# Optimization experiments

Measured on AMD Instinct MI355X. Metric: run time of the kernel, lower is better.

Reference implementation:

```python
import jax, jax.numpy as jnp
import numpy as np

T, B = 512, 64
DIM_INPUT, DIM_LATENT, VOCAB = 512, 1024, 50257


def setup_inputs() -> dict:
    key = jax.random.key(0)
    ks = jax.random.split(key, 12)
    s = 0.02
    return {
        "X": jax.random.randint(ks[0], (T, B), 0, VOCAB, dtype=jnp.int32),
        "h": jax.random.normal(ks[1], (B, DIM_LATENT), dtype=jnp.float32),
        "emb": jax.random.normal(ks[2], (VOCAB, DIM_INPUT), dtype=jnp.float32) * s,
        "Wf": jax.random.normal(ks[3], (DIM_LATENT + DIM_INPUT, DIM_LATENT), dtype=jnp.float32) * s,
        "bf": jnp.zeros((DIM_LATENT,), dtype=jnp.float32),
        "Wi": jax.random.normal(ks[4], (DIM_LATENT + DIM_INPUT, DIM_LATENT), dtype=jnp.float32) * s,
        "bi": jnp.zeros((DIM_LATENT,), dtype=jnp.float32),
        "Wc": jax.random.normal(ks[5], (DIM_LATENT + DIM_INPUT, DIM_LATENT), dtype=jnp.float32) * s,
        "bc": jnp.zeros((DIM_LATENT,), dtype=jnp.float32),
        "Wo": jax.random.normal(ks[6], (DIM_LATENT + DIM_INPUT, DIM_LATENT), dtype=jnp.float32) * s,
        "bo": jnp.zeros((DIM_LATENT,), dtype=jnp.float32),
    }


def reference(X, h, emb, Wf, bf, Wi, bi, Wc, bc, Wo, bo):
    # X: [T, B] int tokens; h: [B, dim_latent]
    xe = emb[X]  # [T, B, dim_input] embedding gather
    c0 = jnp.zeros_like(h)

    def step(carry, x_t):
        h_prev, c_prev = carry
        m = jnp.concatenate([h_prev, x_t], axis=1)  # [B, dl+di]
        ft = jax.nn.sigmoid(m @ Wf + bf)
        it = jax.nn.sigmoid(m @ Wi + bi)
        ct = ft * c_prev + it * jnp.tanh(m @ Wc + bc)
        ot = jax.nn.sigmoid(m @ Wo + bo)
        ht = ot * jnp.tanh(ct)
        return (ht, ct), ht

    (_, _), H = jax.lax.scan(step, (h, c0), xe)
    return H  # [T, B, dim_latent]
```

## Files before the change

### kernel.cpp

```cpp
#include <hip/hip_runtime.h>


namespace {
constexpr int T_STEPS = 512;
constexpr int BATCH   = 64;
constexpr int DI      = 512;
constexpr int DL      = 1024;
constexpr int NKC     = 48;
constexpr int NKC_H   = 32;
constexpr int NBLK    = 256;
constexpr int NTHR    = 320;
constexpr int FPAD    = 32;
constexpr int EPOCH_IDX = NBLK * FPAD;
}

typedef __attribute__((ext_vector_type(8))) short bf16x8;
typedef __attribute__((ext_vector_type(8))) unsigned short u16x8;
typedef __attribute__((ext_vector_type(4))) float f32x4;
typedef __attribute__((ext_vector_type(4))) unsigned int u32x4;
typedef __attribute__((ext_vector_type(2))) unsigned int u32x2;

__device__ __forceinline__ unsigned short f2bf(float x){
  unsigned int u = __float_as_uint(x);
  return (unsigned short)((u + 0x7FFFu + ((u >> 16) & 1u)) >> 16);
}
__device__ __forceinline__ float bf2f(unsigned short b){
  return __uint_as_float(((unsigned int)b) << 16);
}
__device__ __forceinline__ float fast_sigmoid(float v){
  return __fdividef(1.f, 1.f + __expf(-v));
}
__device__ __forceinline__ float fast_tanh(float v){
  v = fminf(fmaxf(v, -15.f), 15.f);
  float t = __expf(2.f * v);
  return __fdividef(t - 1.f, t + 1.f);
}

__global__ void prep_xe(const int* __restrict__ X, const float* __restrict__ emb,
                        unsigned short* __restrict__ xe){
  int i = blockIdx.x * blockDim.x + threadIdx.x;
  const int total = T_STEPS * BATCH * DI / 8;
  if (i >= total) return;
  int row = i >> 6;
  int seg = i & 63;
  int tok = X[row];
  const float* src = emb + (long long)tok * DI + seg * 8;
  float4 v0 = *(const float4*)src;
  float4 v1 = *(const float4*)(src + 4);
  u16x8 o;
  o[0]=f2bf(v0.x); o[1]=f2bf(v0.y); o[2]=f2bf(v0.z); o[3]=f2bf(v0.w);
  o[4]=f2bf(v1.x); o[5]=f2bf(v1.y); o[6]=f2bf(v1.z); o[7]=f2bf(v1.w);
  *(u16x8*)(xe + (long long)row * DI + seg * 8) = o;
}

__global__ void prep_w(const float* __restrict__ Wf, const float* __restrict__ Wi,
                       const float* __restrict__ Wc, const float* __restrict__ Wo,
                       unsigned short* __restrict__ W_hi, unsigned short* __restrict__ W_lo){
  int idx = blockIdx.x * blockDim.x + threadIdx.x;
  if (idx >= 256 * NKC * 64) return;
  int lane = idx & 63;
  int kc   = (idx >> 6) % NKC;
  int bk   = idx / (64 * NKC);
  int lc = lane & 15, kg = lane >> 4;
  int g  = lc >> 2;
  int jl = bk * 4 + (lc & 3);
  const float* Wg = (g == 0) ? Wf : ((g == 1) ? Wi : ((g == 2) ? Wc : Wo));
  int kbase = kc * 32 + kg * 8;
  u16x8 hi, lo;
#pragma unroll
  for (int j = 0; j < 8; j++){
    float wv = Wg[(long long)(kbase + j) * DL + jl];
    unsigned short h = f2bf(wv);
    hi[j] = h;
    lo[j] = f2bf(wv - bf2f(h));
  }
  *(u16x8*)(W_hi + ((long long)(bk * NKC + kc) * 64 + lane) * 8) = hi;
  if (kc < NKC_H)
    *(u16x8*)(W_lo + ((long long)(bk * NKC_H + kc) * 64 + lane) * 8) = lo;
}

__global__ void prep_h(const float* __restrict__ h0,
                       const float* __restrict__ bf_, const float* __restrict__ bi_,
                       const float* __restrict__ bc_, const float* __restrict__ bo_,
                       unsigned short* __restrict__ hRing,
                       float* __restrict__ bias_pack, unsigned int* __restrict__ bar){
  int i = blockIdx.x * blockDim.x + threadIdx.x;
  if (i < BATCH * DL) hRing[i] = f2bf(h0[i]);
  if (i < 4096){
    int r = i & 3, g = (i >> 2) & 3, bk = i >> 4;
    const float* bg = (g == 0) ? bf_ : ((g == 1) ? bi_ : ((g == 2) ? bc_ : bo_));
    bias_pack[i] = bg[bk * 4 + r];
  }
  if (i < (NBLK + 1) * FPAD) bar[i] = 0u;
}

template<bool CACHED>
__launch_bounds__(NTHR, 1)
__global__ void lstm_persist(const unsigned short* __restrict__ xe,
                             const unsigned short* __restrict__ W_hi,
                             const unsigned short* __restrict__ W_lo,
                             unsigned short* __restrict__ hRing,
                             const float* __restrict__ bias_pack,
                             float* __restrict__ out,
                             unsigned int* __restrict__ bar){
  extern __shared__ unsigned short lds[];
  unsigned short* lds_hi = lds;
  unsigned short* lds_lo = lds + NKC * 512;
  __shared__ unsigned short stage_h[BATCH * 4];
  __shared__ float          stage_o[BATCH * 4];
  const int tid  = threadIdx.x;
  const int bk   = blockIdx.x;
  const int w    = tid >> 6;
  const int lane = tid & 63;
  const bool isAgg     = (bk == 0) && (w == 4);
  const bool isCompute = (w < 4);

  const uint4* srcHi = (const uint4*)(W_hi + (size_t)bk * NKC * 512);
  uint4* dHi = (uint4*)lds_hi;
  for (int i = tid; i < 3072; i += NTHR) dHi[i] = srcHi[i];
  const uint4* srcLo = (const uint4*)(W_lo + (size_t)bk * NKC_H * 512);
  uint4* dLo = (uint4*)lds_lo;
  for (int i = tid; i < 2048; i += NTHR) dLo[i] = srcLo[i];
  __syncthreads();

  const int lc = lane & 15;
  const int kg = lane >> 4;
  const int g  = lc >> 2;
  const int rowb = (w << 4) + lc;
  const float bias = bias_pack[bk * 16 + lc];
  const int srcBase = (lane & 48) | (lc & 3);
  const int hOff = rowb * DL + kg * 8;
  const int xOff = rowb * DI + kg * 8;
  unsigned int* epochp = bar + EPOCH_IDX;
  float cr0 = 0.f, cr1 = 0.f, cr2 = 0.f, cr3 = 0.f;

  f32x4 acc0 = {0.f,0.f,0.f,0.f}, acc1 = {0.f,0.f,0.f,0.f};
  f32x4 acc2 = {0.f,0.f,0.f,0.f}, acc3 = {0.f,0.f,0.f,0.f};

#define XSTEP(KC, ACC) {                                                        \
    bf16x8 ax = *(const bf16x8*)(xRow + (KC) * 32);                             \
    bf16x8 bh = *(const bf16x8*)(lds_hi + (NKC_H + (KC)) * 512 + lane * 8);     \
    ACC = __builtin_amdgcn_mfma_f32_16x16x32_bf16(ax, bh, ACC, 0, 0, 0); }
#define HSTEP2(KC, ACC) {                                                       \
    bf16x8 ah = *(const bf16x8*)&hv[KC];                                        \
    bf16x8 bh = *(const bf16x8*)(lds_hi + (KC) * 512 + lane * 8);               \
    bf16x8 bl = *(const bf16x8*)(lds_lo + (KC) * 512 + lane * 8);               \
    ACC = __builtin_amdgcn_mfma_f32_16x16x32_bf16(ah, bh, ACC, 0, 0, 0);        \
    ACC = __builtin_amdgcn_mfma_f32_16x16x32_bf16(ah, bl, ACC, 0, 0, 0); }
#define LOADHC(I, OFFSTR)                                                       \
    asm volatile("global_load_dwordx4 %0, %1, off offset:" OFFSTR               \
                 : "=v"(hv[I]) : "v"(hbase));
#define LOADHU(I, OFFSTR)                                                       \
    asm volatile("global_load_dwordx4 %0, %1, off offset:" OFFSTR " sc0 sc1"    \
                 : "=v"(hv[I]) : "v"(hbase));

  if (isCompute){
    const unsigned short* xRow = xe + xOff;
#pragma unroll
    for (int kc = 0; kc < 16; kc += 4){
      XSTEP(kc, acc0) XSTEP(kc + 1, acc1) XSTEP(kc + 2, acc2) XSTEP(kc + 3, acc3)
    }
  }

#pragma unroll 1
  for (int t = 0; t < T_STEPS; ++t){
    if (t > 0){
      if (isAgg){
        const unsigned tgt = (unsigned)t;
        int spin = 0;
        for (;;){
          unsigned v0 = __hip_atomic_load(bar + (lane      ) * FPAD, __ATOMIC_RELAXED, __HIP_MEMORY_SCOPE_AGENT);
          unsigned v1 = __hip_atomic_load(bar + (lane +  64) * FPAD, __ATOMIC_RELAXED, __HIP_MEMORY_SCOPE_AGENT);
          unsigned v2 = __hip_atomic_load(bar + (lane + 128) * FPAD, __ATOMIC_RELAXED, __HIP_MEMORY_SCOPE_AGENT);
          unsigned v3 = __hip_atomic_load(bar + (lane + 192) * FPAD, __ATOMIC_RELAXED, __HIP_MEMORY_SCOPE_AGENT);
          bool ok = (v0 >= tgt) & (v1 >= tgt) & (v2 >= tgt) & (v3 >= tgt);
          if (__all(ok ? 1 : 0)) break;
          __builtin_amdgcn_s_sleep(1);
          if (++spin > (1 << 15)) break;
        }
        if (lane == 0)
          __hip_atomic_store(epochp, tgt, __ATOMIC_RELAXED, __HIP_MEMORY_SCOPE_AGENT);
      } else if (w == 0){
        const unsigned tgt = (unsigned)t;
        int spin = 0;
        while (__hip_atomic_load(epochp, __ATOMIC_RELAXED, __HIP_MEMORY_SCOPE_AGENT) < tgt){
          __builtin_amdgcn_s_sleep(1);
          if (++spin > (1 << 16)) break;
        }
      }
    }
    __syncthreads();

    const int slotR = CACHED ? t       : (t & 1);
    const int slotW = CACHED ? (t + 1) : ((t + 1) & 1);
    unsigned short* hWr = hRing + (size_t)slotW * (BATCH * DL);
    float* out_t = out + (size_t)t * (BATCH * DL);

    if (isCompute){
      u32x4 hv[32];
      const unsigned short* hbase = hRing + (size_t)slotR * (BATCH * DL) + hOff;
      if constexpr (CACHED){
        LOADHC( 0,"0")    LOADHC( 1,"64")   LOADHC( 2,"128")  LOADHC( 3,"192")
        LOADHC( 4,"256")  LOADHC( 5,"320")  LOADHC( 6,"384")  LOADHC( 7,"448")
        LOADHC( 8,"512")  LOADHC( 9,"576")  LOADHC(10,"640")  LOADHC(11,"704")
        LOADHC(12,"768")  LOADHC(13,"832")  LOADHC(14,"896")  LOADHC(15,"960")
        LOADHC(16,"1024") LOADHC(17,"1088") LOADHC(18,"1152") LOADHC(19,"1216")
        LOADHC(20,"1280") LOADHC(21,"1344") LOADHC(22,"1408") LOADHC(23,"1472")
        LOADHC(24,"1536") LOADHC(25,"1600") LOADHC(26,"1664") LOADHC(27,"1728")
        LOADHC(28,"1792") LOADHC(29,"1856") LOADHC(30,"1920") LOADHC(31,"1984")
      } else {
        LOADHU( 0,"0")    LOADHU( 1,"64")   LOADHU( 2,"128")  LOADHU( 3,"192")
        LOADHU( 4,"256")  LOADHU( 5,"320")  LOADHU( 6,"384")  LOADHU( 7,"448")
        LOADHU( 8,"512")  LOADHU( 9,"576")  LOADHU(10,"640")  LOADHU(11,"704")
        LOADHU(12,"768")  LOADHU(13,"832")  LOADHU(14,"896")  LOADHU(15,"960")
        LOADHU(16,"1024") LOADHU(17,"1088") LOADHU(18,"1152") LOADHU(19,"1216")
        LOADHU(20,"1280") LOADHU(21,"1344") LOADHU(22,"1408") LOADHU(23,"1472")
        LOADHU(24,"1536") LOADHU(25,"1600") LOADHU(26,"1664") LOADHU(27,"1728")
        LOADHU(28,"1792") LOADHU(29,"1856") LOADHU(30,"1920") LOADHU(31,"1984")
      }
      asm volatile("s_waitcnt vmcnt(0)" ::: "memory");
      __builtin_amdgcn_sched_barrier(0);

#pragma unroll
      for (int kc = 0; kc < NKC_H; kc += 4){
        HSTEP2(kc, acc0) HSTEP2(kc + 1, acc1) HSTEP2(kc + 2, acc2) HSTEP2(kc + 3, acc3)
      }
      f32x4 acc = (acc0 + acc1) + (acc2 + acc3);

      float creg[4] = {cr0, cr1, cr2, cr3};
#pragma unroll
      for (int r = 0; r < 4; r++){
        float v = acc[r] + bias;
        float vF = __shfl(v, srcBase);
        float vI = __shfl(v, srcBase + 4);
        float vC = __shfl(v, srcBase + 8);
        float vO = __shfl(v, srcBase + 12);
        if (g == 0){
          int b = (w << 4) | (kg << 2) | r;
          float ft = fast_sigmoid(vF);
          float it = fast_sigmoid(vI);
          float gt = fast_tanh(vC);
          float ot = fast_sigmoid(vO);
          float cn = ft * creg[r] + it * gt;
          creg[r] = cn;
          float hn = ot * fast_tanh(cn);
          int si = (b << 2) | (lc & 3);
          stage_h[si] = f2bf(hn);
          stage_o[si] = hn;
        }
      }
      cr0 = creg[0]; cr1 = creg[1]; cr2 = creg[2]; cr3 = creg[3];
    }

    __syncthreads();

    if (w == 0){
      u32x2  hv2 = *(const u32x2*)&stage_h[lane << 2];
      f32x4  ov  = *(const f32x4*)&stage_o[lane << 2];
      *(float4*)(out_t + lane * DL + (bk << 2)) = *(const float4*)&ov;
      unsigned short* hdst = hWr + lane * DL + (bk << 2);
      asm volatile("global_store_dwordx2 %0, %1, off sc0 sc1"
                   :: "v"(hdst), "v"(hv2) : "memory");
      asm volatile("s_waitcnt vmcnt(0)" ::: "memory");
      __builtin_amdgcn_sched_barrier(0);
      if (tid == 0)
        __hip_atomic_store(bar + bk * FPAD, (unsigned)(t + 1),
                           __ATOMIC_RELAXED, __HIP_MEMORY_SCOPE_AGENT);
    }

    acc0 = (f32x4){0.f,0.f,0.f,0.f}; acc1 = (f32x4){0.f,0.f,0.f,0.f};
    acc2 = (f32x4){0.f,0.f,0.f,0.f}; acc3 = (f32x4){0.f,0.f,0.f,0.f};
    if (isCompute && t + 1 < T_STEPS){
      const unsigned short* xRow = xe + (size_t)(t + 1) * BATCH * DI + xOff;
#pragma unroll
      for (int kc = 0; kc < 16; kc += 4){
        XSTEP(kc, acc0) XSTEP(kc + 1, acc1) XSTEP(kc + 2, acc2) XSTEP(kc + 3, acc3)
      }
    }
  }
#undef XSTEP
#undef HSTEP2
#undef LOADHC
#undef LOADHU
}

extern "C" void kernel_launch(void* const* d_in, const int* in_sizes, int n_in,
                              void* d_out, int out_size, void* d_ws, size_t ws_size,
                              hipStream_t stream){
  const int*   X   = (const int*)d_in[0];
  const float* h0  = (const float*)d_in[1];
  const float* emb = (const float*)d_in[2];
  const float* Wf  = (const float*)d_in[3];
  const float* bf_ = (const float*)d_in[4];
  const float* Wi  = (const float*)d_in[5];
  const float* bi_ = (const float*)d_in[6];
  const float* Wc  = (const float*)d_in[7];
  const float* bc_ = (const float*)d_in[8];
  const float* Wo  = (const float*)d_in[9];
  const float* bo_ = (const float*)d_in[10];
  float* out = (float*)d_out;

  const size_t SLOT = (size_t)BATCH * DL;
  const size_t base_need =
      sizeof(unsigned short) * ((size_t)T_STEPS * BATCH * DI
                              + (size_t)256 * NKC * 512
                              + (size_t)256 * NKC_H * 512)
    + sizeof(float) * 4096
    + sizeof(unsigned int) * (NBLK + 1) * FPAD + 4096;
  const size_t ring_full = sizeof(unsigned short) * SLOT * (size_t)(T_STEPS + 1);
  const bool cached = ws_size >= base_need + ring_full;
  const size_t ring_elems = cached ? SLOT * (size_t)(T_STEPS + 1) : SLOT * 2;

  char* ws = (char*)d_ws;
  size_t off = 0;
  auto alloc = [&](size_t bytes) -> void* {
    void* p = ws + off;
    off = (off + bytes + 255) & ~((size_t)255);
    return p;
  };
  unsigned short* xe        = (unsigned short*)alloc(sizeof(unsigned short) * (size_t)T_STEPS * BATCH * DI);
  unsigned short* W_hi      = (unsigned short*)alloc(sizeof(unsigned short) * (size_t)256 * NKC * 512);
  unsigned short* W_lo      = (unsigned short*)alloc(sizeof(unsigned short) * (size_t)256 * NKC_H * 512);
  unsigned short* hRing     = (unsigned short*)alloc(sizeof(unsigned short) * ring_elems);
  float*          bias_pack = (float*)alloc(sizeof(float) * 4096);
  unsigned int*   bar       = (unsigned int*)alloc(sizeof(unsigned int) * (NBLK + 1) * FPAD);
  (void)in_sizes; (void)n_in; (void)out_size;

  static bool attr_set = false;
  if (!attr_set){
    hipFuncSetAttribute((const void*)lstm_persist<true>,
                        hipFuncAttributeMaxDynamicSharedMemorySize, 160 * 1024);
    hipFuncSetAttribute((const void*)lstm_persist<false>,
                        hipFuncAttributeMaxDynamicSharedMemorySize, 160 * 1024);
    attr_set = true;
  }

  hipLaunchKernelGGL(prep_xe, dim3(8192), dim3(256), 0, stream, X, emb, xe);
  hipLaunchKernelGGL(prep_w,  dim3(3072), dim3(256), 0, stream, Wf, Wi, Wc, Wo, W_hi, W_lo);
  hipLaunchKernelGGL(prep_h,  dim3(256),  dim3(256), 0, stream, h0, bf_, bi_, bc_, bo_,
                     hRing, bias_pack, bar);
  if (cached)
    hipLaunchKernelGGL((lstm_persist<true>),  dim3(NBLK), dim3(NTHR), 80 * 1024, stream,
                       xe, W_hi, W_lo, hRing, bias_pack, out, bar);
  else
    hipLaunchKernelGGL((lstm_persist<false>), dim3(NBLK), dim3(NTHR), 80 * 1024, stream,
                       xe, W_hi, W_lo, hRing, bias_pack, out, bar);
}
```

Measured before the change: 4.355 ms.

## Use a dedicated store/barrier wave with LDS counter instead of block syncs

Wave 4 becomes a dedicated communicator: it waits on an LDS atomic counter that the compute waves bump, then stores h and the output and publishes the per-block flag. Block 0's wave 4 also aggregates the grid barrier. Compute waves no longer run __syncthreads; they only spin on the epoch word, so the output store and barrier overlap with the next step's x-projection. The h ring layout changes to a block-major slot (bk, batch, 4) so each store is contiguous, with loads reshaped as paired dwordx2 reads. This relies on correct workgroup fence ordering between the compute waves and the communicator wave.

```diff
diff --git a/kernel.cpp b/kernel.cpp
--- a/kernel.cpp
+++ b/kernel.cpp
@@ -11,7 +11,9 @@
 constexpr int NBLK    = 256;
 constexpr int NTHR    = 320;
 constexpr int FPAD    = 32;
-constexpr int EPOCH_IDX = NBLK * FPAD;
+constexpr int EPOCH_IDX   = NBLK * FPAD;
+constexpr int SLOT_ELEMS  = NBLK * BATCH * 4;
+constexpr int SLOT_BYTES  = SLOT_ELEMS * 2;
 }
 
 typedef __attribute__((ext_vector_type(8))) short bf16x8;
@@ -85,7 +87,13 @@
                        unsigned short* __restrict__ hRing,
                        float* __restrict__ bias_pack, unsigned int* __restrict__ bar){
   int i = blockIdx.x * blockDim.x + threadIdx.x;
-  if (i < BATCH * DL) hRing[i] = f2bf(h0[i]);
+  if (i < NBLK * BATCH){
+    int bk = i >> 6, b = i & 63;
+    float4 v = *(const float4*)(h0 + (size_t)b * DL + (bk << 2));
+    u16x8* dummy; (void)dummy;
+    unsigned short* d = hRing + (size_t)i * 4;
+    d[0] = f2bf(v.x); d[1] = f2bf(v.y); d[2] = f2bf(v.z); d[3] = f2bf(v.w);
+  }
   if (i < 4096){
     int r = i & 3, g = (i >> 2) & 3, bk = i >> 4;
     const float* bg = (g == 0) ? bf_ : ((g == 1) ? bi_ : ((g == 2) ? bc_ : bo_));
@@ -108,12 +116,11 @@
   unsigned short* lds_lo = lds + NKC * 512;
   __shared__ unsigned short stage_h[BATCH * 4];
   __shared__ float          stage_o[BATCH * 4];
+  __shared__ unsigned int   cnt1;
   const int tid  = threadIdx.x;
   const int bk   = blockIdx.x;
   const int w    = tid >> 6;
   const int lane = tid & 63;
-  const bool isAgg     = (bk == 0) && (w == 4);
-  const bool isCompute = (w < 4);
 
   const uint4* srcHi = (const uint4*)(W_hi + (size_t)bk * NKC * 512);
   uint4* dHi = (uint4*)lds_hi;
@@ -121,7 +128,60 @@
   const uint4* srcLo = (const uint4*)(W_lo + (size_t)bk * NKC_H * 512);
   uint4* dLo = (uint4*)lds_lo;
   for (int i = tid; i < 2048; i += NTHR) dLo[i] = srcLo[i];
+  if (tid == 0) cnt1 = 0u;
   __syncthreads();
+
+  unsigned int* epochp = bar + EPOCH_IDX;
+
+  if (w == 4){
+#pragma unroll 1
+    for (int t = 0; t < T_STEPS; ++t){
+      {
+        const unsigned tgt = 4u * (unsigned)(t + 1);
+        int sp = 0;
+        while (__hip_atomic_load(&cnt1, __ATOMIC_RELAXED, __HIP_MEMORY_SCOPE_WORKGROUP) < tgt){
+          if (++sp > (1 << 22)) break;
+        }
+      }
+      __builtin_amdgcn_fence(__ATOMIC_ACQUIRE, "workgroup");
+
+      const int slotW = CACHED ? (t + 1) : ((t + 1) & 1);
+      u32x2 hv2 = *(const u32x2*)&stage_h[lane << 2];
+      f32x4 ov  = *(const f32x4*)&stage_o[lane << 2];
+      unsigned long long sbR = (unsigned long long)hRing
+                             + (unsigned long long)slotW * SLOT_BYTES + (unsigned)(bk << 9);
+      unsigned voR = (unsigned)(lane << 3);
+      unsigned long long sbO = (unsigned long long)(out + (size_t)t * (BATCH * DL) + (bk << 2));
+      unsigned voO = (unsigned)(lane << 12);
+      asm volatile("global_store_dwordx2 %0, %1, %2 sc0 sc1"
+                   :: "v"(voR), "v"(hv2), "s"(sbR) : "memory");
+      asm volatile("global_store_dwordx4 %0, %1, %2"
+                   :: "v"(voO), "v"(ov), "s"(sbO) : "memory");
+      asm volatile("s_waitcnt vmcnt(1)" ::: "memory");
+      __builtin_amdgcn_sched_barrier(0);
+      if (lane == 0)
+        __hip_atomic_store(bar + bk * FPAD, (unsigned)(t + 1),
+                           __ATOMIC_RELAXED, __HIP_MEMORY_SCOPE_AGENT);
+
+      if (bk == 0 && t + 1 < T_STEPS){
+        const unsigned tg2 = (unsigned)(t + 1);
+        int sp = 0;
+        for (;;){
+          unsigned v0 = __hip_atomic_load(bar + (lane      ) * FPAD, __ATOMIC_RELAXED, __HIP_MEMORY_SCOPE_AGENT);
+          unsigned v1 = __hip_atomic_load(bar + (lane +  64) * FPAD, __ATOMIC_RELAXED, __HIP_MEMORY_SCOPE_AGENT);
+          unsigned v2 = __hip_atomic_load(bar + (lane + 128) * FPAD, __ATOMIC_RELAXED, __HIP_MEMORY_SCOPE_AGENT);
+          unsigned v3 = __hip_atomic_load(bar + (lane + 192) * FPAD, __ATOMIC_RELAXED, __HIP_MEMORY_SCOPE_AGENT);
+          bool ok = (v0 >= tg2) & (v1 >= tg2) & (v2 >= tg2) & (v3 >= tg2);
+          if (__all(ok ? 1 : 0)) break;
+          __builtin_amdgcn_s_sleep(1);
+          if (++sp > (1 << 15)) break;
+        }
+        if (lane == 0)
+          __hip_atomic_store(epochp, tg2, __ATOMIC_RELAXED, __HIP_MEMORY_SCOPE_AGENT);
+      }
+    }
+    return;
+  }
 
   const int lc = lane & 15;
   const int kg = lane >> 4;
@@ -129,9 +189,8 @@
   const int rowb = (w << 4) + lc;
   const float bias = bias_pack[bk * 16 + lc];
   const int srcBase = (lane & 48) | (lc & 3);
-  const int hOff = rowb * DL + kg * 8;
+  const unsigned laneoff = (unsigned)(kg * 1024 + rowb * 8);
   const int xOff = rowb * DI + kg * 8;
-  unsigned int* epochp = bar + EPOCH_IDX;
   float cr0 = 0.f, cr1 = 0.f, cr2 = 0.f, cr3 = 0.f;
 
   f32x4 acc0 = {0.f,0.f,0.f,0.f}, acc1 = {0.f,0.f,0.f,0.f};
@@ -141,20 +200,28 @@
     bf16x8 ax = *(const bf16x8*)(xRow + (KC) * 32);                             \
     bf16x8 bh = *(const bf16x8*)(lds_hi + (NKC_H + (KC)) * 512 + lane * 8);     \
     ACC = __builtin_amdgcn_mfma_f32_16x16x32_bf16(ax, bh, ACC, 0, 0, 0); }
+#define LOADH(KC) { unsigned vo = laneoff + (KC) * 4096u;                       \
+    if constexpr (CACHED){                                                      \
+      asm volatile("global_load_dwordx2 %0, %2, %3\n\t"                         \
+                   "global_load_dwordx2 %1, %2, %3 offset:512"                  \
+                   : "=&v"(hv[(KC)*2]), "=&v"(hv[(KC)*2+1])                     \
+                   : "v"(vo), "s"(sb));                                         \
+    } else {                                                                    \
+      asm volatile("global_load_dwordx2 %0, %2, %3 sc0 sc1\n\t"                 \
+                   "global_load_dwordx2 %1, %2, %3 offset:512 sc0 sc1"          \
+                   : "=&v"(hv[(KC)*2]), "=&v"(hv[(KC)*2+1])                     \
+                   : "v"(vo), "s"(sb));                                         \
+    } }
 #define HSTEP2(KC, ACC) {                                                       \
-    bf16x8 ah = *(const bf16x8*)&hv[KC];                                        \
+    u32x4 av; av[0] = hv[(KC)*2][0]; av[1] = hv[(KC)*2][1];                     \
+    av[2] = hv[(KC)*2+1][0]; av[3] = hv[(KC)*2+1][1];                           \
+    bf16x8 ah = *(bf16x8*)&av;                                                  \
     bf16x8 bh = *(const bf16x8*)(lds_hi + (KC) * 512 + lane * 8);               \
     bf16x8 bl = *(const bf16x8*)(lds_lo + (KC) * 512 + lane * 8);               \
     ACC = __builtin_amdgcn_mfma_f32_16x16x32_bf16(ah, bh, ACC, 0, 0, 0);        \
     ACC = __builtin_amdgcn_mfma_f32_16x16x32_bf16(ah, bl, ACC, 0, 0, 0); }
-#define LOADHC(I, OFFSTR)                                                       \
-    asm volatile("global_load_dwordx4 %0, %1, off offset:" OFFSTR               \
-                 : "=v"(hv[I]) : "v"(hbase));
-#define LOADHU(I, OFFSTR)                                                       \
-    asm volatile("global_load_dwordx4 %0, %1, off offset:" OFFSTR " sc0 sc1"    \
-                 : "=v"(hv[I]) : "v"(hbase));
-
-  if (isCompute){
+
+  {
     const unsigned short* xRow = xe + xOff;
 #pragma unroll
     for (int kc = 0; kc < 16; kc += 4){
@@ -165,112 +232,64 @@
 #pragma unroll 1
   for (int t = 0; t < T_STEPS; ++t){
     if (t > 0){
-      if (isAgg){
-        const unsigned tgt = (unsigned)t;
-        int spin = 0;
-        for (;;){
-          unsigned v0 = __hip_atomic_load(bar + (lane      ) * FPAD, __ATOMIC_RELAXED, __HIP_MEMORY_SCOPE_AGENT);
-          unsigned v1 = __hip_atomic_load(bar + (lane +  64) * FPAD, __ATOMIC_RELAXED, __HIP_MEMORY_SCOPE_AGENT);
-          unsigned v2 = __hip_atomic_load(bar + (lane + 128) * FPAD, __ATOMIC_RELAXED, __HIP_MEMORY_SCOPE_AGENT);
-          unsigned v3 = __hip_atomic_load(bar + (lane + 192) * FPAD, __ATOMIC_RELAXED, __HIP_MEMORY_SCOPE_AGENT);
-          bool ok = (v0 >= tgt) & (v1 >= tgt) & (v2 >= tgt) & (v3 >= tgt);
-          if (__all(ok ? 1 : 0)) break;
-          __builtin_amdgcn_s_sleep(1);
-          if (++spin > (1 << 15)) break;
-        }
-        if (lane == 0)
-          __hip_atomic_store(epochp, tgt, __ATOMIC_RELAXED, __HIP_MEMORY_SCOPE_AGENT);
-      } else if (w == 0){
-        const unsigned tgt = (unsigned)t;
-        int spin = 0;
-        while (__hip_atomic_load(epochp, __ATOMIC_RELAXED, __HIP_MEMORY_SCOPE_AGENT) < tgt){
-          __builtin_amdgcn_s_sleep(1);
-          if (++spin > (1 << 16)) break;
-        }
-      }
-    }
-    __syncthreads();
-
-    const int slotR = CACHED ? t       : (t & 1);
-    const int slotW = CACHED ? (t + 1) : ((t + 1) & 1);
-    unsigned short* hWr = hRing + (size_t)slotW * (BATCH * DL);
-    float* out_t = out + (size_t)t * (BATCH * DL);
-
-    if (isCompute){
-      u32x4 hv[32];
-      const unsigned short* hbase = hRing + (size_t)slotR * (BATCH * DL) + hOff;
-      if constexpr (CACHED){
-        LOADHC( 0,"0")    LOADHC( 1,"64")   LOADHC( 2,"128")  LOADHC( 3,"192")
-        LOADHC( 4,"256")  LOADHC( 5,"320")  LOADHC( 6,"384")  LOADHC( 7,"448")
-        LOADHC( 8,"512")  LOADHC( 9,"576")  LOADHC(10,"640")  LOADHC(11,"704")
-        LOADHC(12,"768")  LOADHC(13,"832")  LOADHC(14,"896")  LOADHC(15,"960")
-        LOADHC(16,"1024") LOADHC(17,"1088") LOADHC(18,"1152") LOADHC(19,"1216")
-        LOADHC(20,"1280") LOADHC(21,"1344") LOADHC(22,"1408") LOADHC(23,"1472")
-        LOADHC(24,"1536") LOADHC(25,"1600") LOADHC(26,"1664") LOADHC(27,"1728")
-        LOADHC(28,"1792") LOADHC(29,"1856") LOADHC(30,"1920") LOADHC(31,"1984")
-      } else {
-        LOADHU( 0,"0")    LOADHU( 1,"64")   LOADHU( 2,"128")  LOADHU( 3,"192")
-        LOADHU( 4,"256")  LOADHU( 5,"320")  LOADHU( 6,"384")  LOADHU( 7,"448")
-        LOADHU( 8,"512")  LOADHU( 9,"576")  LOADHU(10,"640")  LOADHU(11,"704")
-        LOADHU(12,"768")  LOADHU(13,"832")  LOADHU(14,"896")  LOADHU(15,"960")
-        LOADHU(16,"1024") LOADHU(17,"1088") LOADHU(18,"1152") LOADHU(19,"1216")
-        LOADHU(20,"1280") LOADHU(21,"1344") LOADHU(22,"1408") LOADHU(23,"1472")
-        LOADHU(24,"1536") LOADHU(25,"1600") LOADHU(26,"1664") LOADHU(27,"1728")
-        LOADHU(28,"1792") LOADHU(29,"1856") LOADHU(30,"1920") LOADHU(31,"1984")
-      }
-      asm volatile("s_waitcnt vmcnt(0)" ::: "memory");
-      __builtin_amdgcn_sched_barrier(0);
-
-#pragma unroll
-      for (int kc = 0; kc < NKC_H; kc += 4){
-        HSTEP2(kc, acc0) HSTEP2(kc + 1, acc1) HSTEP2(kc + 2, acc2) HSTEP2(kc + 3, acc3)
-      }
-      f32x4 acc = (acc0 + acc1) + (acc2 + acc3);
-
-      float creg[4] = {cr0, cr1, cr2, cr3};
-#pragma unroll
-      for (int r = 0; r < 4; r++){
-        float v = acc[r] + bias;
-        float vF = __shfl(v, srcBase);
-        float vI = __shfl(v, srcBase + 4);
-        float vC = __shfl(v, srcBase + 8);
-        float vO = __shfl(v, srcBase + 12);
-        if (g == 0){
-          int b = (w << 4) | (kg << 2) | r;
-          float ft = fast_sigmoid(vF);
-          float it = fast_sigmoid(vI);
-          float gt = fast_tanh(vC);
-          float ot = fast_sigmoid(vO);
-          float cn = ft * creg[r] + it * gt;
-          creg[r] = cn;
-          float hn = ot * fast_tanh(cn);
-          int si = (b << 2) | (lc & 3);
-          stage_h[si] = f2bf(hn);
-          stage_o[si] = hn;
-        }
-      }
-      cr0 = creg[0]; cr1 = creg[1]; cr2 = creg[2]; cr3 = creg[3];
-    }
-
-    __syncthreads();
-
-    if (w == 0){
-      u32x2  hv2 = *(const u32x2*)&stage_h[lane << 2];
-      f32x4  ov  = *(const f32x4*)&stage_o[lane << 2];
-      *(float4*)(out_t + lane * DL + (bk << 2)) = *(const float4*)&ov;
-      unsigned short* hdst = hWr + lane * DL + (bk << 2);
-      asm volatile("global_store_dwordx2 %0, %1, off sc0 sc1"
-                   :: "v"(hdst), "v"(hv2) : "memory");
-      asm volatile("s_waitcnt vmcnt(0)" ::: "memory");
-      __builtin_amdgcn_sched_barrier(0);
-      if (tid == 0)
-        __hip_atomic_store(bar + bk * FPAD, (unsigned)(t + 1),
-                           __ATOMIC_RELAXED, __HIP_MEMORY_SCOPE_AGENT);
-    }
+      const unsigned tgt = (unsigned)t;
+      int sp = 0;
+      while (__hip_atomic_load(epochp, __ATOMIC_RELAXED, __HIP_MEMORY_SCOPE_AGENT) < tgt){
+        __builtin_amdgcn_s_sleep(1);
+        if (++sp > (1 << 16)) break;
+      }
+    }
+    asm volatile("" ::: "memory");
+
+    const int slotR = CACHED ? t : (t & 1);
+    unsigned long long sb = (unsigned long long)hRing
+                          + (unsigned long long)slotR * SLOT_BYTES;
+
+    u32x2 hv[64];
+    LOADH( 0) LOADH( 1) LOADH( 2) LOADH( 3) LOADH( 4) LOADH( 5) LOADH( 6) LOADH( 7)
+    LOADH( 8) LOADH( 9) LOADH(10) LOADH(11) LOADH(12) LOADH(13) LOADH(14) LOADH(15)
+    LOADH(16) LOADH(17) LOADH(18) LOADH(19) LOADH(20) LOADH(21) LOADH(22) LOADH(23)
+    LOADH(24) LOADH(25) LOADH(26) LOADH(27) LOADH(28) LOADH(29) LOADH(30) LOADH(31)
+    asm volatile("s_waitcnt vmcnt(0)" ::: "memory");
+    __builtin_amdgcn_sched_barrier(0);
+
+#pragma unroll
+    for (int kc = 0; kc < NKC_H; kc += 4){
+      HSTEP2(kc, acc0) HSTEP2(kc + 1, acc1) HSTEP2(kc + 2, acc2) HSTEP2(kc + 3, acc3)
+    }
+    f32x4 acc = (acc0 + acc1) + (acc2 + acc3);
+
+    float creg[4] = {cr0, cr1, cr2, cr3};
+#pragma unroll
+    for (int r = 0; r < 4; r++){
+      float v = acc[r] + bias;
+      float vF = __shfl(v, srcBase);
+      float vI = __shfl(v, srcBase + 4);
+      float vC = __shfl(v, srcBase + 8);
+      float vO = __shfl(v, srcBase + 12);
+      if (g == 0){
+        int b = (w << 4) | (kg << 2) | r;
+        float ft = fast_sigmoid(vF);
+        float it = fast_sigmoid(vI);
+        float gt = fast_tanh(vC);
+        float ot = fast_sigmoid(vO);
+        float cn = ft * creg[r] + it * gt;
+        creg[r] = cn;
+        float hn = ot * fast_tanh(cn);
+        int si = (b << 2) | (lc & 3);
+        stage_h[si] = f2bf(hn);
+        stage_o[si] = hn;
+      }
+    }
+    cr0 = creg[0]; cr1 = creg[1]; cr2 = creg[2]; cr3 = creg[3];
+
+    __builtin_amdgcn_fence(__ATOMIC_RELEASE, "workgroup");
+    if (lane == 0)
+      __hip_atomic_fetch_add(&cnt1, 1u, __ATOMIC_RELAXED, __HIP_MEMORY_SCOPE_WORKGROUP);
 
     acc0 = (f32x4){0.f,0.f,0.f,0.f}; acc1 = (f32x4){0.f,0.f,0.f,0.f};
     acc2 = (f32x4){0.f,0.f,0.f,0.f}; acc3 = (f32x4){0.f,0.f,0.f,0.f};
-    if (isCompute && t + 1 < T_STEPS){
+    if (t + 1 < T_STEPS){
       const unsigned short* xRow = xe + (size_t)(t + 1) * BATCH * DI + xOff;
 #pragma unroll
       for (int kc = 0; kc < 16; kc += 4){
@@ -279,9 +298,8 @@
     }
   }
 #undef XSTEP
+#undef LOADH
 #undef HSTEP2
-#undef LOADHC
-#undef LOADHU
 }
 
 extern "C" void kernel_launch(void* const* d_in, const int* in_sizes, int n_in,
@@ -300,16 +318,15 @@
   const float* bo_ = (const float*)d_in[10];
   float* out = (float*)d_out;
 
-  const size_t SLOT = (size_t)BATCH * DL;
   const size_t base_need =
       sizeof(unsigned short) * ((size_t)T_STEPS * BATCH * DI
                               + (size_t)256 * NKC * 512
                               + (size_t)256 * NKC_H * 512)
     + sizeof(float) * 4096
     + sizeof(unsigned int) * (NBLK + 1) * FPAD + 4096;
-  const size_t ring_full = sizeof(unsigned short) * SLOT * (size_t)(T_STEPS + 1);
+  const size_t ring_full = (size_t)SLOT_BYTES * (size_t)(T_STEPS + 1);
   const bool cached = ws_size >= base_need + ring_full;
-  const size_t ring_elems = cached ? SLOT * (size_t)(T_STEPS + 1) : SLOT * 2;
+  const size_t ring_bytes = cached ? ring_full : (size_t)SLOT_BYTES * 2;
 
   char* ws = (char*)d_ws;
   size_t off = 0;
@@ -321,7 +338,7 @@
   unsigned short* xe        = (unsigned short*)alloc(sizeof(unsigned short) * (size_t)T_STEPS * BATCH * DI);
   unsigned short* W_hi      = (unsigned short*)alloc(sizeof(unsigned short) * (size_t)256 * NKC * 512);
   unsigned short* W_lo      = (unsigned short*)alloc(sizeof(unsigned short) * (size_t)256 * NKC_H * 512);
-  unsigned short* hRing     = (unsigned short*)alloc(sizeof(unsigned short) * ring_elems);
+  unsigned short* hRing     = (unsigned short*)alloc(ring_bytes);
   float*          bias_pack = (float*)alloc(sizeof(float) * 4096);
   unsigned int*   bar       = (unsigned int*)alloc(sizeof(unsigned int) * (NBLK + 1) * FPAD);
   (void)in_sizes; (void)n_in; (void)out_size;
```

Result: slower. 5.984 ms (+37.4%).

## Replace aggregator-wave grid barrier with single atomic counter barrier

Applied to the files above, without the earlier changes.

Removes the dedicated aggregator wave in block 0 that polled per-block flags and published an epoch. Each block now atomically increments one global counter after writing h, and wave 0 of each block spins until the counter reaches NBLK*t. Thread count drops to 256 because the extra wave is gone. This cuts one hop of latency per step from the barrier chain, at the cost of 256 atomics contending on a single address and all blocks polling that same line.

```diff
diff --git a/kernel.cpp b/kernel.cpp
--- a/kernel.cpp
+++ b/kernel.cpp
@@ -9,9 +9,8 @@
 constexpr int NKC     = 48;
 constexpr int NKC_H   = 32;
 constexpr int NBLK    = 256;
-constexpr int NTHR    = 320;
+constexpr int NTHR    = 256;
 constexpr int FPAD    = 32;
-constexpr int EPOCH_IDX = NBLK * FPAD;
 }
 
 typedef __attribute__((ext_vector_type(8))) short bf16x8;
@@ -91,7 +90,7 @@
     const float* bg = (g == 0) ? bf_ : ((g == 1) ? bi_ : ((g == 2) ? bc_ : bo_));
     bias_pack[i] = bg[bk * 4 + r];
   }
-  if (i < (NBLK + 1) * FPAD) bar[i] = 0u;
+  if (i < 8 * FPAD) bar[i] = 0u;
 }
 
 template<bool CACHED>
@@ -112,8 +111,6 @@
   const int bk   = blockIdx.x;
   const int w    = tid >> 6;
   const int lane = tid & 63;
-  const bool isAgg     = (bk == 0) && (w == 4);
-  const bool isCompute = (w < 4);
 
   const uint4* srcHi = (const uint4*)(W_hi + (size_t)bk * NKC * 512);
   uint4* dHi = (uint4*)lds_hi;
@@ -131,7 +128,6 @@
   const int srcBase = (lane & 48) | (lc & 3);
   const int hOff = rowb * DL + kg * 8;
   const int xOff = rowb * DI + kg * 8;
-  unsigned int* epochp = bar + EPOCH_IDX;
   float cr0 = 0.f, cr1 = 0.f, cr2 = 0.f, cr3 = 0.f;
 
   f32x4 acc0 = {0.f,0.f,0.f,0.f}, acc1 = {0.f,0.f,0.f,0.f};
@@ -154,7 +150,7 @@
     asm volatile("global_load_dwordx4 %0, %1, off offset:" OFFSTR " sc0 sc1"    \
                  : "=v"(hv[I]) : "v"(hbase));
 
-  if (isCompute){
+  {
     const unsigned short* xRow = xe + xOff;
 #pragma unroll
     for (int kc = 0; kc < 16; kc += 4){
@@ -164,29 +160,12 @@
 
 #pragma unroll 1
   for (int t = 0; t < T_STEPS; ++t){
-    if (t > 0){
-      if (isAgg){
-        const unsigned tgt = (unsigned)t;
-        int spin = 0;
-        for (;;){
-          unsigned v0 = __hip_atomic_load(bar + (lane      ) * FPAD, __ATOMIC_RELAXED, __HIP_MEMORY_SCOPE_AGENT);
-          unsigned v1 = __hip_atomic_load(bar + (lane +  64) * FPAD, __ATOMIC_RELAXED, __HIP_MEMORY_SCOPE_AGENT);
-          unsigned v2 = __hip_atomic_load(bar + (lane + 128) * FPAD, __ATOMIC_RELAXED, __HIP_MEMORY_SCOPE_AGENT);
-          unsigned v3 = __hip_atomic_load(bar + (lane + 192) * FPAD, __ATOMIC_RELAXED, __HIP_MEMORY_SCOPE_AGENT);
-          bool ok = (v0 >= tgt) & (v1 >= tgt) & (v2 >= tgt) & (v3 >= tgt);
-          if (__all(ok ? 1 : 0)) break;
-          __builtin_amdgcn_s_sleep(1);
-          if (++spin > (1 << 15)) break;
-        }
-        if (lane == 0)
-          __hip_atomic_store(epochp, tgt, __ATOMIC_RELAXED, __HIP_MEMORY_SCOPE_AGENT);
-      } else if (w == 0){
-        const unsigned tgt = (unsigned)t;
-        int spin = 0;
-        while (__hip_atomic_load(epochp, __ATOMIC_RELAXED, __HIP_MEMORY_SCOPE_AGENT) < tgt){
-          __builtin_amdgcn_s_sleep(1);
-          if (++spin > (1 << 16)) break;
-        }
+    if (t > 0 && w == 0){
+      const unsigned tgt = (unsigned)NBLK * (unsigned)t;
+      int spin = 0;
+      while (__hip_atomic_load(bar, __ATOMIC_RELAXED, __HIP_MEMORY_SCOPE_AGENT) < tgt){
+        __builtin_amdgcn_s_sleep(1);
+        if (++spin > (1 << 16)) break;
       }
     }
     __syncthreads();
@@ -196,61 +175,59 @@
     unsigned short* hWr = hRing + (size_t)slotW * (BATCH * DL);
     float* out_t = out + (size_t)t * (BATCH * DL);
 
-    if (isCompute){
-      u32x4 hv[32];
-      const unsigned short* hbase = hRing + (size_t)slotR * (BATCH * DL) + hOff;
-      if constexpr (CACHED){
-        LOADHC( 0,"0")    LOADHC( 1,"64")   LOADHC( 2,"128")  LOADHC( 3,"192")
-        LOADHC( 4,"256")  LOADHC( 5,"320")  LOADHC( 6,"384")  LOADHC( 7,"448")
-        LOADHC( 8,"512")  LOADHC( 9,"576")  LOADHC(10,"640")  LOADHC(11,"704")
-        LOADHC(12,"768")  LOADHC(13,"832")  LOADHC(14,"896")  LOADHC(15,"960")
-        LOADHC(16,"1024") LOADHC(17,"1088") LOADHC(18,"1152") LOADHC(19,"1216")
-        LOADHC(20,"1280") LOADHC(21,"1344") LOADHC(22,"1408") LOADHC(23,"1472")
-        LOADHC(24,"1536") LOADHC(25,"1600") LOADHC(26,"1664") LOADHC(27,"1728")
-        LOADHC(28,"1792") LOADHC(29,"1856") LOADHC(30,"1920") LOADHC(31,"1984")
-      } else {
-        LOADHU( 0,"0")    LOADHU( 1,"64")   LOADHU( 2,"128")  LOADHU( 3,"192")
-        LOADHU( 4,"256")  LOADHU( 5,"320")  LOADHU( 6,"384")  LOADHU( 7,"448")
-        LOADHU( 8,"512")  LOADHU( 9,"576")  LOADHU(10,"640")  LOADHU(11,"704")
-        LOADHU(12,"768")  LOADHU(13,"832")  LOADHU(14,"896")  LOADHU(15,"960")
-        LOADHU(16,"1024") LOADHU(17,"1088") LOADHU(18,"1152") LOADHU(19,"1216")
-        LOADHU(20,"1280") LOADHU(21,"1344") LOADHU(22,"1408") LOADHU(23,"1472")
-        LOADHU(24,"1536") LOADHU(25,"1600") LOADHU(26,"1664") LOADHU(27,"1728")
-        LOADHU(28,"1792") LOADHU(29,"1856") LOADHU(30,"1920") LOADHU(31,"1984")
+    u32x4 hv[32];
+    const unsigned short* hbase = hRing + (size_t)slotR * (BATCH * DL) + hOff;
+    if constexpr (CACHED){
+      LOADHC( 0,"0")    LOADHC( 1,"64")   LOADHC( 2,"128")  LOADHC( 3,"192")
+      LOADHC( 4,"256")  LOADHC( 5,"320")  LOADHC( 6,"384")  LOADHC( 7,"448")
+      LOADHC( 8,"512")  LOADHC( 9,"576")  LOADHC(10,"640")  LOADHC(11,"704")
+      LOADHC(12,"768")  LOADHC(13,"832")  LOADHC(14,"896")  LOADHC(15,"960")
+      LOADHC(16,"1024") LOADHC(17,"1088") LOADHC(18,"1152") LOADHC(19,"1216")
+      LOADHC(20,"1280") LOADHC(21,"1344") LOADHC(22,"1408") LOADHC(23,"1472")
+      LOADHC(24,"1536") LOADHC(25,"1600") LOADHC(26,"1664") LOADHC(27,"1728")
+      LOADHC(28,"1792") LOADHC(29,"1856") LOADHC(30,"1920") LOADHC(31,"1984")
+    } else {
+      LOADHU( 0,"0")    LOADHU( 1,"64")   LOADHU( 2,"128")  LOADHU( 3,"192")
+      LOADHU( 4,"256")  LOADHU( 5,"320")  LOADHU( 6,"384")  LOADHU( 7,"448")
+      LOADHU( 8,"512")  LOADHU( 9,"576")  LOADHU(10,"640")  LOADHU(11,"704")
+      LOADHU(12,"768")  LOADHU(13,"832")  LOADHU(14,"896")  LOADHU(15,"960")
+      LOADHU(16,"1024") LOADHU(17,"1088") LOADHU(18,"1152") LOADHU(19,"1216")
+      LOADHU(20,"1280") LOADHU(21,"1344") LOADHU(22,"1408") LOADHU(23,"1472")
+      LOADHU(24,"1536") LOADHU(25,"1600") LOADHU(26,"1664") LOADHU(27,"1728")
+      LOADHU(28,"1792") LOADHU(29,"1856") LOADHU(30,"1920") LOADHU(31,"1984")
+    }
+    asm volatile("s_waitcnt vmcnt(0)" ::: "memory");
+    __builtin_amdgcn_sched_barrier(0);
+
+#pragma unroll
+    for (int kc = 0; kc < NKC_H; kc += 4){
+      HSTEP2(kc, acc0) HSTEP2(kc + 1, acc1) HSTEP2(kc + 2, acc2) HSTEP2(kc + 3, acc3)
+    }
+    f32x4 acc = (acc0 + acc1) + (acc2 + acc3);
+
+    float creg[4] = {cr0, cr1, cr2, cr3};
+#pragma unroll
+    for (int r = 0; r < 4; r++){
+      float v = acc[r] + bias;
+      float vF = __shfl(v, srcBase);
+      float vI = __shfl(v, srcBase + 4);
+      float vC = __shfl(v, srcBase + 8);
+      float vO = __shfl(v, srcBase + 12);
+      if (g == 0){
+        int b = (w << 4) | (kg << 2) | r;
+        float ft = fast_sigmoid(vF);
+        float it = fast_sigmoid(vI);
+        float gt = fast_tanh(vC);
+        float ot = fast_sigmoid(vO);
+        float cn = ft * creg[r] + it * gt;
+        creg[r] = cn;
+        float hn = ot * fast_tanh(cn);
+        int si = (b << 2) | (lc & 3);
+        stage_h[si] = f2bf(hn);
+        stage_o[si] = hn;
       }
-      asm volatile("s_waitcnt vmcnt(0)" ::: "memory");
-      __builtin_amdgcn_sched_barrier(0);
-
-#pragma unroll
-      for (int kc = 0; kc < NKC_H; kc += 4){
-        HSTEP2(kc, acc0) HSTEP2(kc + 1, acc1) HSTEP2(kc + 2, acc2) HSTEP2(kc + 3, acc3)
-      }
-      f32x4 acc = (acc0 + acc1) + (acc2 + acc3);
-
-      float creg[4] = {cr0, cr1, cr2, cr3};
-#pragma unroll
-      for (int r = 0; r < 4; r++){
-        float v = acc[r] + bias;
-        float vF = __shfl(v, srcBase);
-        float vI = __shfl(v, srcBase + 4);
-        float vC = __shfl(v, srcBase + 8);
-        float vO = __shfl(v, srcBase + 12);
-        if (g == 0){
-          int b = (w << 4) | (kg << 2) | r;
-          float ft = fast_sigmoid(vF);
-          float it = fast_sigmoid(vI);
-          float gt = fast_tanh(vC);
-          float ot = fast_sigmoid(vO);
-          float cn = ft * creg[r] + it * gt;
-          creg[r] = cn;
-          float hn = ot * fast_tanh(cn);
-          int si = (b << 2) | (lc & 3);
-          stage_h[si] = f2bf(hn);
-          stage_o[si] = hn;
-        }
-      }
-      cr0 = creg[0]; cr1 = creg[1]; cr2 = creg[2]; cr3 = creg[3];
-    }
+    }
+    cr0 = creg[0]; cr1 = creg[1]; cr2 = creg[2]; cr3 = creg[3];
 
     __syncthreads();
 
@@ -264,13 +241,12 @@
       asm volatile("s_waitcnt vmcnt(0)" ::: "memory");
       __builtin_amdgcn_sched_barrier(0);
       if (tid == 0)
-        __hip_atomic_store(bar + bk * FPAD, (unsigned)(t + 1),
-                           __ATOMIC_RELAXED, __HIP_MEMORY_SCOPE_AGENT);
+        __hip_atomic_fetch_add(bar, 1u, __ATOMIC_RELAXED, __HIP_MEMORY_SCOPE_AGENT);
     }
 
     acc0 = (f32x4){0.f,0.f,0.f,0.f}; acc1 = (f32x4){0.f,0.f,0.f,0.f};
     acc2 = (f32x4){0.f,0.f,0.f,0.f}; acc3 = (f32x4){0.f,0.f,0.f,0.f};
-    if (isCompute && t + 1 < T_STEPS){
+    if (t + 1 < T_STEPS){
       const unsigned short* xRow = xe + (size_t)(t + 1) * BATCH * DI + xOff;
 #pragma unroll
       for (int kc = 0; kc < 16; kc += 4){
@@ -306,7 +282,7 @@
                               + (size_t)256 * NKC * 512
                               + (size_t)256 * NKC_H * 512)
     + sizeof(float) * 4096
-    + sizeof(unsigned int) * (NBLK + 1) * FPAD + 4096;
+    + sizeof(unsigned int) * 8 * FPAD + 4096;
   const size_t ring_full = sizeof(unsigned short) * SLOT * (size_t)(T_STEPS + 1);
   const bool cached = ws_size >= base_need + ring_full;
   const size_t ring_elems = cached ? SLOT * (size_t)(T_STEPS + 1) : SLOT * 2;
@@ -323,7 +299,7 @@
   unsigned short* W_lo      = (unsigned short*)alloc(sizeof(unsigned short) * (size_t)256 * NKC_H * 512);
   unsigned short* hRing     = (unsigned short*)alloc(sizeof(unsigned short) * ring_elems);
   float*          bias_pack = (float*)alloc(sizeof(float) * 4096);
-  unsigned int*   bar       = (unsigned int*)alloc(sizeof(unsigned int) * (NBLK + 1) * FPAD);
+  unsigned int*   bar       = (unsigned int*)alloc(sizeof(unsigned int) * 8 * FPAD);
   (void)in_sizes; (void)n_in; (void)out_size;
 
   static bool attr_set = false;
```

Result: slower. 4.905 ms (+12.6%).
